# Optimization experiments

Hardware: AMD Instinct MI355X
Metric: run time of the kernel (lower is better)

Reference implementation:

```python
import jax, jax.numpy as jnp
import numpy as np

N = 50000   # nodes per branch
E = 500000  # edges per branch
B = 256     # graphs per batch
F = 320     # node feature dim = num_features_xd*10
H = 10      # GAT heads
C = 32      # GAT out channels per head
NEG_SLOPE = 0.2


def _seg_sum(x, idx, n):
    return jax.ops.segment_sum(x, idx, num_segments=n)


def gcn_conv(x, edge_index, W, b):
    n = x.shape[0]
    h = x @ W  # [N, F]
    loop = jnp.arange(n, dtype=edge_index.dtype)
    src = jnp.concatenate([edge_index[0], loop])
    dst = jnp.concatenate([edge_index[1], loop])
    deg = _seg_sum(jnp.ones_like(dst, dtype=h.dtype), dst, n)
    dinv = jnp.where(deg > 0, jax.lax.rsqrt(deg), 0.0)
    coef = (dinv[src] * dinv[dst])[:, None]  # [E+N, 1]
    out = _seg_sum(h[src] * coef, dst, n)
    return out + b


def gat_conv(x, edge_index, W, att_src, att_dst, b):
    # PyG GATConv, heads=H, concat=True, add_self_loops=True, negative_slope=0.2
    n = x.shape[0]
    h = (x @ W).reshape(n, H, C)  # [N, H, C]
    a_s = jnp.sum(h * att_src, axis=-1)  # [N, H]
    a_d = jnp.sum(h * att_dst, axis=-1)  # [N, H]
    loop = jnp.arange(n, dtype=edge_index.dtype)
    src = jnp.concatenate([edge_index[0], loop])
    dst = jnp.concatenate([edge_index[1], loop])
    e = jax.nn.leaky_relu(a_s[src] + a_d[dst], NEG_SLOPE)  # [E+N, H]
    m = jax.ops.segment_max(e, dst, num_segments=n)  # neighborhood max per head
    p = jnp.exp(e - m[dst])
    denom = _seg_sum(p, dst, n)  # [N, H], >0 thanks to self loops
    alpha = p / denom[dst]
    out = _seg_sum(h[src] * alpha[:, :, None], dst, n)  # [N, H, C]
    return out.reshape(n, H * C) + b


def graph_branch(x, edge_index, batch, params):
    x = jax.nn.relu(gcn_conv(x, edge_index, params['W_gcn'], params['b_gcn']))
    x = jax.nn.relu(gat_conv(x, edge_index, params['W_gat'], params['att_src'], params['att_dst'], params['b_gat']))
    gmp = jax.ops.segment_max(x, batch, num_segments=B)  # [B, F]
    cnt = _seg_sum(jnp.ones((x.shape[0], 1), x.dtype), batch, B)
    gap = _seg_sum(x, batch, B) / jnp.maximum(cnt, 1.0)
    g = jnp.concatenate([gmp, gap], axis=1)  # [B, 2F]
    g = jax.nn.relu(g @ params['W_fc_g1'] + params['b_fc_g1'])
    # dropout is identity in eval mode
    g = g @ params['W_fc_g2'] + params['b_fc_g2']
    return g


def _forward(x_a, x_b, edge_index_a, edge_index_b, batch_a, batch_b, params):
    ga = graph_branch(x_a, edge_index_a, batch_a, params)
    gb = graph_branch(x_b, edge_index_b, batch_b, params)
    xc = jnp.concatenate([ga, gb], axis=1)  # [B, 256]
    xc = jax.nn.relu(xc @ params['W_fc1'] + params['b_fc1'])
    xc = jax.nn.relu(xc @ params['W_fc2'] + params['b_fc2'])
    return xc @ params['W_out'] + params['b_out']  # [B, 2]


def setup_inputs() -> dict:
    key = jax.random.key(0)
    ks = jax.random.split(key, 24)
    s = 0.05
    d = {
        'x_a': jax.random.normal(ks[0], (N, F), jnp.float32),
        'x_b': jax.random.normal(ks[1], (N, F), jnp.float32),
        'edge_index_a': jax.random.randint(ks[2], (2, E), 0, N, jnp.int32),
        'edge_index_b': jax.random.randint(ks[3], (2, E), 0, N, jnp.int32),
        'batch_a': jnp.sort(jax.random.randint(ks[4], (N,), 0, B, jnp.int32)),
        'batch_b': jnp.sort(jax.random.randint(ks[5], (N,), 0, B, jnp.int32)),
        'W_gcn': jax.random.normal(ks[6], (F, F), jnp.float32) * s,
        'b_gcn': jax.random.normal(ks[7], (F,), jnp.float32) * s,
        'W_gat': jax.random.normal(ks[8], (F, H * C), jnp.float32) * s,
        'att_src': jax.random.normal(ks[9], (H, C), jnp.float32) * s,
        'att_dst': jax.random.normal(ks[10], (H, C), jnp.float32) * s,
        'b_gat': jax.random.normal(ks[11], (H * C,), jnp.float32) * s,
        'W_fc_g1': jax.random.normal(ks[12], (2 * F, 1500), jnp.float32) * s,
        'b_fc_g1': jax.random.normal(ks[13], (1500,), jnp.float32) * s,
        'W_fc_g2': jax.random.normal(ks[14], (1500, 128), jnp.float32) * s,
        'b_fc_g2': jax.random.normal(ks[15], (128,), jnp.float32) * s,
        'W_fc1': jax.random.normal(ks[16], (256, 1024), jnp.float32) * s,
        'b_fc1': jax.random.normal(ks[17], (1024,), jnp.float32) * s,
        'W_fc2': jax.random.normal(ks[18], (1024, 512), jnp.float32) * s,
        'b_fc2': jax.random.normal(ks[19], (512,), jnp.float32) * s,
        'W_out': jax.random.normal(ks[20], (512, 2), jnp.float32) * s,
        'b_out': jax.random.normal(ks[21], (2,), jnp.float32) * s,
    }
    return d


def reference(x_a, x_b, edge_index_a, edge_index_b, batch_a, batch_b,
              W_gcn, b_gcn, W_gat, att_src, att_dst, b_gat,
              W_fc_g1, b_fc_g1, W_fc_g2, b_fc_g2,
              W_fc1, b_fc1, W_fc2, b_fc2, W_out, b_out):
    params = dict(W_gcn=W_gcn, b_gcn=b_gcn, W_gat=W_gat, att_src=att_src,
                  att_dst=att_dst, b_gat=b_gat, W_fc_g1=W_fc_g1, b_fc_g1=b_fc_g1,
                  W_fc_g2=W_fc_g2, b_fc_g2=b_fc_g2, W_fc1=W_fc1, b_fc1=b_fc1,
                  W_fc2=W_fc2, b_fc2=b_fc2, W_out=W_out, b_out=b_out)
    return _forward(x_a, x_b, edge_index_a, edge_index_b, batch_a, batch_b, params)
```

## Files before the change

kernel.cpp:

```cpp
#include <hip/hip_runtime.h>
#include <type_traits>

#define FDIM 320
#define NHEADS 10
#define NGR 256

typedef __bf16 bf16x8 __attribute__((ext_vector_type(8)));
typedef float f32x4 __attribute__((ext_vector_type(4)));

__global__ void wconv2_kernel(const float* __restrict__ Wg, const float* __restrict__ Wa,
                              __bf16* __restrict__ Tg, __bf16* __restrict__ Ta) {
  int idx = blockIdx.x * 256 + threadIdx.x;
  bool first = idx < FDIM * FDIM;
  const float* W = first ? Wg : Wa;
  __bf16* T = first ? Tg : Ta;
  int i2 = first ? idx : idx - FDIM * FDIM;
  int k = i2 / FDIM, c = i2 - k * FDIM;
  T[c * FDIM + k] = (__bf16)W[i2];
}

#define GLSTR 40

template<typename TA, bool SCORES>
__global__ __launch_bounds__(256, 2) void gemm320v3_kernel(
    const TA* __restrict__ A, const TA* __restrict__ A2, int Npad, int Nreal,
    const __bf16* __restrict__ Wt, __bf16* __restrict__ C,
    const float* __restrict__ att_s, const float* __restrict__ att_d,
    float* __restrict__ as_, float* __restrict__ ad_)
{
  __shared__ __bf16 As[2][64 * GLSTR];
  __shared__ __bf16 Bs[2][320 * GLSTR];

  const int tid = threadIdx.x;
  const int lane = tid & 63;
  const int w = tid >> 6;
  const int wr = w >> 1, wc = w & 1;
  const int r = lane & 15, kg = lane >> 4;
  const int m0 = blockIdx.x * 64;
  const bool brB = m0 >= Npad;
  const int loff = brB ? Npad : 0;

  const int brow = tid >> 2, bq = tid & 3;
  const int grow = m0 + brow;
  const int lrow = grow - loff;
  const bool arow_ok = lrow < Nreal;

  bf16x8 bstg[5];
  bf16x8 astg;
  float4 af32a, af32b;

  auto stage_load = [&](int k0) {
    #pragma unroll
    for (int i = 0; i < 5; i++) {
      int ch = tid + i * 256;
      int col = ch >> 2, kc = ch & 3;
      bstg[i] = *(const bf16x8*)(Wt + (size_t)col * FDIM + k0 + kc * 8);
    }
    if constexpr (std::is_same_v<TA, float>) {
      if (arow_ok) {
        const float* Ab = brB ? A2 : A;
        const float4* ap = (const float4*)(Ab + (size_t)lrow * FDIM + k0 + bq * 8);
        af32a = ap[0]; af32b = ap[1];
      }
    } else {
      if (arow_ok) astg = *(const bf16x8*)(A + (size_t)grow * FDIM + k0 + bq * 8);
    }
  };
  auto stage_write = [&](int b) {
    #pragma unroll
    for (int i = 0; i < 5; i++) {
      int ch = tid + i * 256;
      int col = ch >> 2, kc = ch & 3;
      *(bf16x8*)&Bs[b][col * GLSTR + kc * 8] = bstg[i];
    }
    bf16x8 v = {};
    if constexpr (std::is_same_v<TA, float>) {
      if (arow_ok) {
        v[0]=(__bf16)af32a.x; v[1]=(__bf16)af32a.y; v[2]=(__bf16)af32a.z; v[3]=(__bf16)af32a.w;
        v[4]=(__bf16)af32b.x; v[5]=(__bf16)af32b.y; v[6]=(__bf16)af32b.z; v[7]=(__bf16)af32b.w;
      }
    } else {
      if (arow_ok) v = astg;
    }
    *(bf16x8*)&As[b][brow * GLSTR + bq * 8] = v;
  };

  f32x4 acc0[10], acc1[10];
  #pragma unroll
  for (int i = 0; i < 10; i++) { acc0[i] = (f32x4){0,0,0,0}; acc1[i] = (f32x4){0,0,0,0}; }

  stage_load(0);
  stage_write(0);
  __syncthreads();

  int cur = 0;
  for (int k = 0; k < 10; k++) {
    if (k < 9) stage_load((k + 1) * 32);
    {
      bf16x8 a0 = *(const bf16x8*)&As[cur][(wr*32 + r)      * GLSTR + kg*8];
      bf16x8 a1 = *(const bf16x8*)&As[cur][(wr*32 + 16 + r) * GLSTR + kg*8];
      #pragma unroll
      for (int nf = 0; nf < 10; nf++) {
        bf16x8 b = *(const bf16x8*)&Bs[cur][(wc*160 + nf*16 + r) * GLSTR + kg*8];
        acc0[nf] = __builtin_amdgcn_mfma_f32_16x16x32_bf16(a0, b, acc0[nf], 0, 0, 0);
        acc1[nf] = __builtin_amdgcn_mfma_f32_16x16x32_bf16(a1, b, acc1[nf], 0, 0, 0);
      }
    }
    if (k < 9) {
      stage_write(cur ^ 1);
      __syncthreads();
      cur ^= 1;
    }
  }

  #pragma unroll
  for (int nf = 0; nf < 10; nf++) {
    int gn = wc*160 + nf*16 + r;
    #pragma unroll
    for (int q = 0; q < 4; q++) {
      int gm0 = m0 + wr*32 + kg*4 + q;
      if (gm0 - loff < Nreal) C[(size_t)gm0 * FDIM + gn] = (__bf16)acc0[nf][q];
      int gm1 = gm0 + 16;
      if (gm1 - loff < Nreal) C[(size_t)gm1 * FDIM + gn] = (__bf16)acc1[nf][q];
    }
  }

  if constexpr (SCORES) {
    #pragma unroll
    for (int th = 0; th < 5; th++) {
      int t = wc * 5 + th;
      float s0 = att_s[t*32 + r],      s1 = att_s[t*32 + 16 + r];
      float d0 = att_d[t*32 + r],      d1 = att_d[t*32 + 16 + r];
      #pragma unroll
      for (int q = 0; q < 4; q++) {
        float ps0 = acc0[2*th][q]*s0 + acc0[2*th+1][q]*s1;
        float ps1 = acc1[2*th][q]*s0 + acc1[2*th+1][q]*s1;
        float pd0 = acc0[2*th][q]*d0 + acc0[2*th+1][q]*d1;
        float pd1 = acc1[2*th][q]*d0 + acc1[2*th+1][q]*d1;
        #pragma unroll
        for (int off = 1; off < 16; off <<= 1) {
          ps0 += __shfl_xor(ps0, off, 16);
          ps1 += __shfl_xor(ps1, off, 16);
          pd0 += __shfl_xor(pd0, off, 16);
          pd1 += __shfl_xor(pd1, off, 16);
        }
        if (r == 0) {
          int row0 = m0 + wr*32 + kg*4 + q;
          if (row0 - loff < Nreal) { as_[row0*NHEADS + t] = ps0; ad_[row0*NHEADS + t] = pd0; }
          int row1 = row0 + 16;
          if (row1 - loff < Nreal) { as_[row1*NHEADS + t] = ps1; ad_[row1*NHEADS + t] = pd1; }
        }
      }
    }
  }
}

#define BM 128
#define BN 64
#define BK 32
#define LSTR 56

template<int FLAGS>
__global__ __launch_bounds__(256) void gemm_bf16_kernel(
    const float* __restrict__ A, const float* __restrict__ B,
    float* __restrict__ C, const float* __restrict__ bias,
    int M, int N, int K, int ldc)
{
  __shared__ __bf16 As[BM * LSTR];
  __shared__ __bf16 Bs[BN * LSTR];

  const int tid = threadIdx.x;
  const int lane = tid & 63;
  const int w = tid >> 6;
  const int wm = w >> 1, wn = w & 1;
  const int r = lane & 15, kg = lane >> 4;
  const int m0 = blockIdx.x * BM, n0 = blockIdx.y * BN;

  f32x4 acc[4][2];
  #pragma unroll
  for (int i = 0; i < 4; i++)
    #pragma unroll
    for (int j = 0; j < 2; j++)
      acc[i][j] = (f32x4){0.f, 0.f, 0.f, 0.f};

  const int arow = tid >> 1, ahalf = tid & 1;
  const int bk = tid >> 3, bn = (tid & 7) * 8;

  for (int k0 = 0; k0 < K; k0 += BK) {
    __syncthreads();
    {
      int gm = m0 + arow;
      int kbase = k0 + ahalf * 16;
      float tmp[16];
      if (gm < M && kbase + 16 <= K) {
        const float4* ap = (const float4*)(A + (size_t)gm * K + kbase);
        #pragma unroll
        for (int q = 0; q < 4; q++) {
          float4 v = ap[q];
          tmp[q*4+0] = v.x; tmp[q*4+1] = v.y; tmp[q*4+2] = v.z; tmp[q*4+3] = v.w;
        }
      } else {
        #pragma unroll
        for (int q = 0; q < 16; q++) {
          int kk = kbase + q;
          tmp[q] = (gm < M && kk < K) ? A[(size_t)gm * K + kk] : 0.f;
        }
      }
      bf16x8 v0, v1;
      #pragma unroll
      for (int q = 0; q < 8; q++) { v0[q] = (__bf16)tmp[q]; v1[q] = (__bf16)tmp[q+8]; }
      bf16x8* dp = (bf16x8*)&As[arow * LSTR + ahalf * 16];
      dp[0] = v0; dp[1] = v1;
    }
    {
      int gk = k0 + bk;
      float tb[8];
      if (gk < K && n0 + bn + 8 <= N) {
        const float4* bp = (const float4*)(B + (size_t)gk * N + n0 + bn);
        float4 u0 = bp[0], u1 = bp[1];
        tb[0]=u0.x; tb[1]=u0.y; tb[2]=u0.z; tb[3]=u0.w;
        tb[4]=u1.x; tb[5]=u1.y; tb[6]=u1.z; tb[7]=u1.w;
      } else {
        #pragma unroll
        for (int q = 0; q < 8; q++) {
          int gn = n0 + bn + q;
          tb[q] = (gk < K && gn < N) ? B[(size_t)gk * N + gn] : 0.f;
        }
      }
      #pragma unroll
      for (int q = 0; q < 8; q++) Bs[(bn + q) * LSTR + bk] = (__bf16)tb[q];
    }
    __syncthreads();
    bf16x8 af[4], bfr[2];
    #pragma unroll
    for (int mf = 0; mf < 4; mf++)
      af[mf] = *(const bf16x8*)&As[(wm*64 + mf*16 + r) * LSTR + kg*8];
    #pragma unroll
    for (int nf = 0; nf < 2; nf++)
      bfr[nf] = *(const bf16x8*)&Bs[(wn*32 + nf*16 + r) * LSTR + kg*8];
    #pragma unroll
    for (int mf = 0; mf < 4; mf++)
      #pragma unroll
      for (int nf = 0; nf < 2; nf++)
        acc[mf][nf] = __builtin_amdgcn_mfma_f32_16x16x32_bf16(af[mf], bfr[nf], acc[mf][nf], 0, 0, 0);
  }

  #pragma unroll
  for (int mf = 0; mf < 4; mf++) {
    #pragma unroll
    for (int nf = 0; nf < 2; nf++) {
      #pragma unroll
      for (int q = 0; q < 4; q++) {
        int gm = m0 + wm*64 + mf*16 + kg*4 + q;
        int gn = n0 + wn*32 + nf*16 + r;
        if (gm < M && gn < N) {
          float v = acc[mf][nf][q];
          if (FLAGS & 2) v += bias[gn];
          if (FLAGS & 1) v = fmaxf(v, 0.f);
          C[(size_t)gm * ldc + gn] = v;
        }
      }
    }
  }
}

__global__ __launch_bounds__(256) void gemm_splitk_kernel(
    const float* __restrict__ A, const float* __restrict__ B,
    float* __restrict__ P, int M, int N, int K, int KS)
{
  __shared__ __bf16 As[BM * LSTR];
  __shared__ __bf16 Bs[BN * LSTR];

  const int tid = threadIdx.x;
  const int lane = tid & 63;
  const int w = tid >> 6;
  const int wm = w >> 1, wn = w & 1;
  const int r = lane & 15, kg = lane >> 4;
  const int m0 = blockIdx.x * BM, n0 = blockIdx.y * BN;
  const int kstart = blockIdx.z * KS;
  const int kend = min(K, kstart + KS);

  f32x4 acc[4][2];
  #pragma unroll
  for (int i = 0; i < 4; i++)
    #pragma unroll
    for (int j = 0; j < 2; j++)
      acc[i][j] = (f32x4){0.f, 0.f, 0.f, 0.f};

  const int arow = tid >> 1, ahalf = tid & 1;
  const int bk = tid >> 3, bn = (tid & 7) * 8;

  for (int k0 = kstart; k0 < kend; k0 += BK) {
    __syncthreads();
    {
      int gm = m0 + arow;
      int kbase = k0 + ahalf * 16;
      float tmp[16];
      if (gm < M && kbase + 16 <= kend) {
        const float4* ap = (const float4*)(A + (size_t)gm * K + kbase);
        #pragma unroll
        for (int q = 0; q < 4; q++) {
          float4 v = ap[q];
          tmp[q*4+0] = v.x; tmp[q*4+1] = v.y; tmp[q*4+2] = v.z; tmp[q*4+3] = v.w;
        }
      } else {
        #pragma unroll
        for (int q = 0; q < 16; q++) {
          int kk = kbase + q;
          tmp[q] = (gm < M && kk < kend) ? A[(size_t)gm * K + kk] : 0.f;
        }
      }
      bf16x8 v0, v1;
      #pragma unroll
      for (int q = 0; q < 8; q++) { v0[q] = (__bf16)tmp[q]; v1[q] = (__bf16)tmp[q+8]; }
      bf16x8* dp = (bf16x8*)&As[arow * LSTR + ahalf * 16];
      dp[0] = v0; dp[1] = v1;
    }
    {
      int gk = k0 + bk;
      float tb[8];
      if (gk < kend && n0 + bn + 8 <= N) {
        const float4* bp = (const float4*)(B + (size_t)gk * N + n0 + bn);
        float4 u0 = bp[0], u1 = bp[1];
        tb[0]=u0.x; tb[1]=u0.y; tb[2]=u0.z; tb[3]=u0.w;
        tb[4]=u1.x; tb[5]=u1.y; tb[6]=u1.z; tb[7]=u1.w;
      } else {
        #pragma unroll
        for (int q = 0; q < 8; q++) {
          int gn = n0 + bn + q;
          tb[q] = (gk < kend && gn < N) ? B[(size_t)gk * N + gn] : 0.f;
        }
      }
      #pragma unroll
      for (int q = 0; q < 8; q++) Bs[(bn + q) * LSTR + bk] = (__bf16)tb[q];
    }
    __syncthreads();
    bf16x8 af[4], bfr[2];
    #pragma unroll
    for (int mf = 0; mf < 4; mf++)
      af[mf] = *(const bf16x8*)&As[(wm*64 + mf*16 + r) * LSTR + kg*8];
    #pragma unroll
    for (int nf = 0; nf < 2; nf++)
      bfr[nf] = *(const bf16x8*)&Bs[(wn*32 + nf*16 + r) * LSTR + kg*8];
    #pragma unroll
    for (int mf = 0; mf < 4; mf++)
      #pragma unroll
      for (int nf = 0; nf < 2; nf++)
        acc[mf][nf] = __builtin_amdgcn_mfma_f32_16x16x32_bf16(af[mf], bfr[nf], acc[mf][nf], 0, 0, 0);
  }

  float* Pp = P + (size_t)blockIdx.z * M * N;
  #pragma unroll
  for (int mf = 0; mf < 4; mf++) {
    #pragma unroll
    for (int nf = 0; nf < 2; nf++) {
      #pragma unroll
      for (int q = 0; q < 4; q++) {
        int gm = m0 + wm*64 + mf*16 + kg*4 + q;
        int gn = n0 + wn*32 + nf*16 + r;
        if (gm < M && gn < N)
          Pp[(size_t)gm * N + gn] = acc[mf][nf][q];
      }
    }
  }
}

template<int FLAGS, bool STACK>
__global__ void reduce_kernel(const float* __restrict__ P, float* __restrict__ C,
                              const float* __restrict__ bias, int M, int N, int S, int ldc)
{
  int i = blockIdx.x * 256 + threadIdx.x;
  if (i >= M * N) return;
  float v = 0.f;
  for (int s = 0; s < S; s++) v += P[(size_t)s * M * N + i];
  int row = i / N, col = i - row * N;
  if (FLAGS & 2) v += bias[col];
  if (FLAGS & 1) v = fmaxf(v, 0.f);
  if (STACK) { if (row >= (M >> 1)) { row -= (M >> 1); col += N; } }
  C[(size_t)row * ldc + col] = v;
}

__global__ void count_kernel(const int* __restrict__ dst_a, const int* __restrict__ dst_b,
                             int* __restrict__ cnt, int E, int Npad) {
  int e = blockIdx.x * 256 + threadIdx.x;
  if (e < E) atomicAdd(&cnt[dst_a[e]], 1);
  else if (e < 2 * E) atomicAdd(&cnt[dst_b[e - E] + Npad], 1);
}

__global__ void bsum_kernel(const int* __restrict__ cnt, int* __restrict__ bsum, int n) {
  __shared__ int wp[4];
  int tid = threadIdx.x, lane = tid & 63, wid = tid >> 6;
  int i = blockIdx.x * 256 + tid;
  int v = (i < n) ? cnt[i] : 0;
  #pragma unroll
  for (int off = 32; off >= 1; off >>= 1) v += __shfl_xor(v, off, 64);
  if (lane == 0) wp[wid] = v;
  __syncthreads();
  if (tid == 0) bsum[blockIdx.x] = wp[0] + wp[1] + wp[2] + wp[3];
}

__global__ __launch_bounds__(1024) void bscan_kernel(int* __restrict__ bsum, int nb) {
  __shared__ int wp[16];
  int tid = threadIdx.x, lane = tid & 63, wid = tid >> 6;
  int v = (tid < nb) ? bsum[tid] : 0;
  int xv = v;
  #pragma unroll
  for (int off = 1; off < 64; off <<= 1) {
    int y = __shfl_up(xv, off, 64);
    if (lane >= off) xv += y;
  }
  if (lane == 63) wp[wid] = xv;
  __syncthreads();
  if (tid == 0) { int s = 0; for (int k = 0; k < 16; k++) { int t = wp[k]; wp[k] = s; s += t; } }
  __syncthreads();
  if (tid < nb) bsum[tid] = wp[wid] + xv - v;
}

__global__ void rpfill_kernel(const int* __restrict__ cnt, const int* __restrict__ bsum,
                              int* __restrict__ rp, float* __restrict__ dinv, int n, int E2) {
  __shared__ int wp[4];
  int tid = threadIdx.x, lane = tid & 63, wid = tid >> 6;
  int i = blockIdx.x * 256 + tid;
  int v = (i < n) ? cnt[i] : 0;
  int xv = v;
  #pragma unroll
  for (int off = 1; off < 64; off <<= 1) {
    int y = __shfl_up(xv, off, 64);
    if (lane >= off) xv += y;
  }
  if (lane == 63) wp[wid] = xv;
  __syncthreads();
  if (tid == 0) { int s = 0; for (int k = 0; k < 4; k++) { int t = wp[k]; wp[k] = s; s += t; } }
  __syncthreads();
  if (i < n) {
    rp[i] = bsum[blockIdx.x] + wp[wid] + xv - v;
    dinv[i] = rsqrtf((float)(v + 1));
  }
  if (blockIdx.x == 0 && tid == 0) rp[n] = E2;
}

__global__ void fill_kernel(const int* __restrict__ sa, const int* __restrict__ da,
                            const int* __restrict__ sb, const int* __restrict__ db,
                            const int* __restrict__ rp, int* __restrict__ fil,
                            int* __restrict__ csr, int E, int Npad) {
  int e = blockIdx.x * 256 + threadIdx.x;
  if (e >= 2 * E) return;
  int s, d;
  if (e < E) { s = sa[e]; d = da[e]; }
  else       { s = sb[e - E] + Npad; d = db[e - E] + Npad; }
  int pos = rp[d] + atomicAdd(&fil[d], 1);
  csr[pos] = s;
}

__global__ void gcn_agg_kernel(const __bf16* __restrict__ h, const int* __restrict__ rp,
                               const int* __restrict__ csr, const float* __restrict__ dinv,
                               const float* __restrict__ bias, __bf16* __restrict__ out,
                               int n2, int Npad, int Nreal)
{
  const int lane = threadIdx.x & 63;
  int v0 = blockIdx.x * 4 + (threadIdx.x >> 6);
  if (v0 >= n2) return;
  const int v = __builtin_amdgcn_readfirstlane(v0);
  const int lv = (v >= Npad) ? v - Npad : v;
  if (lv >= Nreal) return;
  const bool act = lane < 40;
  const float dv = dinv[v];
  const int e0 = rp[v], e1 = rp[v + 1];
  float acc[8], bia[8];
  if (act) {
    bf16x8 hv = *(const bf16x8*)(h + (size_t)v * FDIM + 8 * lane);
    const float4* bp = (const float4*)(bias + 8 * lane);
    float4 b0 = bp[0], b1 = bp[1];
    bia[0]=b0.x; bia[1]=b0.y; bia[2]=b0.z; bia[3]=b0.w;
    bia[4]=b1.x; bia[5]=b1.y; bia[6]=b1.z; bia[7]=b1.w;
    #pragma unroll
    for (int j = 0; j < 8; j++) acc[j] = dv * (float)hv[j];
  }
  int e = e0;
  for (; e + 4 <= e1; e += 4) {
    int sj0 = csr[e], sj1 = csr[e+1], sj2 = csr[e+2], sj3 = csr[e+3];
    float c0 = dinv[sj0], c1 = dinv[sj1], c2 = dinv[sj2], c3 = dinv[sj3];
    if (act) {
      bf16x8 h0 = *(const bf16x8*)(h + (size_t)sj0 * FDIM + 8 * lane);
      bf16x8 h1 = *(const bf16x8*)(h + (size_t)sj1 * FDIM + 8 * lane);
      bf16x8 h2 = *(const bf16x8*)(h + (size_t)sj2 * FDIM + 8 * lane);
      bf16x8 h3 = *(const bf16x8*)(h + (size_t)sj3 * FDIM + 8 * lane);
      #pragma unroll
      for (int j = 0; j < 8; j++)
        acc[j] += c0 * (float)h0[j] + c1 * (float)h1[j]
                + c2 * (float)h2[j] + c3 * (float)h3[j];
    }
  }
  for (; e < e1; e++) {
    int sj = csr[e];
    float cj = dinv[sj];
    if (act) {
      bf16x8 hv = *(const bf16x8*)(h + (size_t)sj * FDIM + 8 * lane);
      #pragma unroll
      for (int j = 0; j < 8; j++) acc[j] += cj * (float)hv[j];
    }
  }
  if (act) {
    bf16x8 o;
    #pragma unroll
    for (int j = 0; j < 8; j++) o[j] = (__bf16)fmaxf(dv * acc[j] + bia[j], 0.f);
    *(bf16x8*)(out + (size_t)v * FDIM + 8 * lane) = o;
  }
}

__device__ __forceinline__ float lrelu(float x) { return x > 0.f ? x : 0.2f * x; }

__global__ void mdenom4_kernel(const int* __restrict__ rp, const int* __restrict__ csr,
                               const float* __restrict__ as_, const float* __restrict__ ad_,
                               float* __restrict__ aint, float* __restrict__ aself,
                               int n2, int Npad, int Nreal)
{
  int tid = blockIdx.x * 256 + threadIdx.x;
  if (tid >= n2 * NHEADS) return;
  int v = tid / NHEADS, t = tid - v * NHEADS;
  int lv = (v >= Npad) ? v - Npad : v;
  if (lv >= Nreal) return;
  int e0 = rp[v], e1 = rp[v + 1];
  float adv = ad_[tid];
  float esf = lrelu(as_[tid] + adv);
  float m = esf, den = 1.f;
  for (int e = e0; e < e1; e++) {
    int s = csr[e];
    float ev = lrelu(as_[s * NHEADS + t] + adv);
    float nm = fmaxf(m, ev);
    den = den * __expf(m - nm) + __expf(ev - nm);
    m = nm;
  }
  float inv = 1.f / den;
  for (int e = e0; e < e1; e++) {
    int s = csr[e];
    aint[(size_t)e * NHEADS + t] = __expf(lrelu(as_[s * NHEADS + t] + adv) - m) * inv;
  }
  aself[tid] = __expf(esf - m) * inv;
}

__global__ void gat_agg_kernel(const __bf16* __restrict__ h, const int* __restrict__ rp,
                               const int* __restrict__ csr, const float* __restrict__ aint,
                               const float* __restrict__ aself, const float* __restrict__ bias,
                               __bf16* __restrict__ out, int n2, int Npad, int Nreal)
{
  const int lane = threadIdx.x & 63;
  int v0 = blockIdx.x * 4 + (threadIdx.x >> 6);
  if (v0 >= n2) return;
  const int v = __builtin_amdgcn_readfirstlane(v0);
  const int lv = (v >= Npad) ? v - Npad : v;
  if (lv >= Nreal) return;
  const bool act = lane < 40;
  const int hl = lane >> 2;
  const int e0 = rp[v], e1 = rp[v + 1];

  float acc[8], bia[8];
  if (act) {
    float aslf = aself[v * NHEADS + hl];
    bf16x8 hv = *(const bf16x8*)(h + (size_t)v * FDIM + 8 * lane);
    const float4* bp = (const float4*)(bias + 8 * lane);
    float4 b0 = bp[0], b1 = bp[1];
    bia[0]=b0.x; bia[1]=b0.y; bia[2]=b0.z; bia[3]=b0.w;
    bia[4]=b1.x; bia[5]=b1.y; bia[6]=b1.z; bia[7]=b1.w;
    #pragma unroll
    for (int j = 0; j < 8; j++) acc[j] = aslf * (float)hv[j];
  }

  int e = e0;
  for (; e + 4 <= e1; e += 4) {
    int sj0 = csr[e], sj1 = csr[e+1], sj2 = csr[e+2], sj3 = csr[e+3];
    if (act) {
      float a0 = aint[(size_t)(e+0) * NHEADS + hl];
      float a1 = aint[(size_t)(e+1) * NHEADS + hl];
      float a2 = aint[(size_t)(e+2) * NHEADS + hl];
      float a3 = aint[(size_t)(e+3) * NHEADS + hl];
      bf16x8 h0 = *(const bf16x8*)(h + (size_t)sj0 * FDIM + 8 * lane);
      bf16x8 h1 = *(const bf16x8*)(h + (size_t)sj1 * FDIM + 8 * lane);
      bf16x8 h2 = *(const bf16x8*)(h + (size_t)sj2 * FDIM + 8 * lane);
      bf16x8 h3 = *(const bf16x8*)(h + (size_t)sj3 * FDIM + 8 * lane);
      #pragma unroll
      for (int j = 0; j < 8; j++)
        acc[j] += a0 * (float)h0[j] + a1 * (float)h1[j]
                + a2 * (float)h2[j] + a3 * (float)h3[j];
    }
  }
  for (; e < e1; e++) {
    int sj = csr[e];
    if (act) {
      float al = aint[(size_t)e * NHEADS + hl];
      bf16x8 hv = *(const bf16x8*)(h + (size_t)sj * FDIM + 8 * lane);
      #pragma unroll
      for (int j = 0; j < 8; j++) acc[j] += al * (float)hv[j];
    }
  }
  if (act) {
    bf16x8 o;
    #pragma unroll
    for (int j = 0; j < 8; j++) o[j] = (__bf16)fmaxf(acc[j] + bia[j], 0.f);
    *(bf16x8*)(out + (size_t)v * FDIM + 8 * lane) = o;
  }
}

__global__ void bstart_kernel(const int* __restrict__ ba, const int* __restrict__ bb,
                              int* __restrict__ bst, int n, int Npad) {
  int idx = blockIdx.x * 256 + threadIdx.x;
  if (idx >= 2 * (n + 1)) return;
  int br = idx >= (n + 1);
  int v = idx - br * (n + 1);
  const int* batch = br ? bb : ba;
  int off = br ? Npad : 0;
  int* bs = bst + br * (NGR + 1);
  int bv = (v < n) ? batch[v] : NGR;
  int bp = (v == 0) ? -1 : batch[v - 1];
  for (int gg = bp + 1; gg <= bv; gg++) bs[gg] = v + off;
}

__global__ __launch_bounds__(256) void pool_kernel(
    const __bf16* __restrict__ xin, const int* __restrict__ bstart,
    float* __restrict__ g)
{
  __shared__ float pmx[4][FDIM];
  __shared__ float psm[4][FDIM];
  const int gid = blockIdx.x;
  const int br = gid >= NGR;
  const int lg = gid - br * NGR;
  const int* bs = bstart + br * (NGR + 1);
  const int lane = threadIdx.x & 63;
  const int wid = threadIdx.x >> 6;
  const bool act = lane < 40;
  const int s = bs[lg], e = bs[lg + 1];
  float mx[8], sm[8];
  #pragma unroll
  for (int j = 0; j < 8; j++) { mx[j] = -__builtin_inff(); sm[j] = 0.f; }
  for (int v = s + wid; v < e; v += 4) {
    if (act) {
      bf16x8 hv = *(const bf16x8*)(xin + (size_t)v * FDIM + 8 * lane);
      #pragma unroll
      for (int j = 0; j < 8; j++) {
        float val = (float)hv[j];
        mx[j] = fmaxf(mx[j], val);
        sm[j] += val;
      }
    }
  }
  if (act) {
    #pragma unroll
    for (int j = 0; j < 8; j++) {
      pmx[wid][8 * lane + j] = mx[j];
      psm[wid][8 * lane + j] = sm[j];
    }
  }
  __syncthreads();
  if (wid == 0 && act) {
    float cntf = (float)(e - s);
    float rcnt = 1.f / fmaxf(cntf, 1.f);
    #pragma unroll
    for (int j = 0; j < 8; j++) {
      int c = 8 * lane + j;
      float m2 = fmaxf(fmaxf(pmx[0][c], pmx[1][c]), fmaxf(pmx[2][c], pmx[3][c]));
      float s2 = psm[0][c] + psm[1][c] + psm[2][c] + psm[3][c];
      g[gid * (2 * FDIM) + c] = m2;
      g[gid * (2 * FDIM) + FDIM + c] = s2 * rcnt;
    }
  }
}

extern "C" void kernel_launch(void* const* d_in, const int* in_sizes, int n_in,
                              void* d_out, int out_size, void* d_ws, size_t ws_size,
                              hipStream_t stream)
{
  const int N = in_sizes[0] / FDIM;
  const int E = in_sizes[2] / 2;
  const int Npad = (N + 63) & ~63;
  const int n2 = 2 * Npad;
  const int NB2 = (n2 + 255) / 256;

  const float* x_a = (const float*)d_in[0];
  const float* x_b = (const float*)d_in[1];
  const int*   ei_a = (const int*)d_in[2];
  const int*   ei_b = (const int*)d_in[3];
  const int*   bat_a = (const int*)d_in[4];
  const int*   bat_b = (const int*)d_in[5];
  const float* W_gcn   = (const float*)d_in[6];
  const float* b_gcn   = (const float*)d_in[7];
  const float* W_gat   = (const float*)d_in[8];
  const float* att_src = (const float*)d_in[9];
  const float* att_dst = (const float*)d_in[10];
  const float* b_gat   = (const float*)d_in[11];
  const float* W_fc_g1 = (const float*)d_in[12];
  const float* b_fc_g1 = (const float*)d_in[13];
  const float* W_fc_g2 = (const float*)d_in[14];
  const float* b_fc_g2 = (const float*)d_in[15];
  const float* W_fc1   = (const float*)d_in[16];
  const float* b_fc1   = (const float*)d_in[17];
  const float* W_fc2   = (const float*)d_in[18];
  const float* b_fc2   = (const float*)d_in[19];
  const float* W_out   = (const float*)d_in[20];
  const float* b_out   = (const float*)d_in[21];
  float* outp = (float*)d_out;

  char* ws = (char*)d_ws;
  size_t off = 0;
  auto alloc = [&](size_t bytes) -> char* {
    char* p = ws + off;
    off += (bytes + 255) & ~(size_t)255;
    return p;
  };
  int*    cnt    = (int*)alloc((size_t)n2 * 4);
  int*    fil    = (int*)alloc((size_t)n2 * 4);
  size_t  zero_span = (size_t)((char*)fil - (char*)cnt) + (((size_t)n2 * 4 + 255) & ~(size_t)255);
  int*    rp     = (int*)alloc((size_t)(n2 + 1) * 4);
  int*    bsum   = (int*)alloc((size_t)NB2 * 4);
  int*    csr    = (int*)alloc((size_t)2 * E * 4);
  float*  dinv   = (float*)alloc((size_t)n2 * 4);
  int*    bstart = (int*)alloc((size_t)2 * (NGR + 1) * 4);
  __bf16* WgcnT  = (__bf16*)alloc((size_t)FDIM * FDIM * 2);
  __bf16* WgatT  = (__bf16*)alloc((size_t)FDIM * FDIM * 2);
  __bf16* hbuf   = (__bf16*)alloc((size_t)n2 * FDIM * 2);
  __bf16* xbuf   = (__bf16*)alloc((size_t)n2 * FDIM * 2);
  float*  as_    = (float*)alloc((size_t)n2 * NHEADS * 4);
  float*  ad_    = (float*)alloc((size_t)n2 * NHEADS * 4);
  float*  aself  = (float*)alloc((size_t)n2 * NHEADS * 4);
  size_t aint_bytes = (size_t)2 * E * NHEADS * 4;
  size_t part_bytes = (size_t)8 * 512 * 512 * 4;
  float*  aint   = (float*)alloc(aint_bytes > part_bytes ? aint_bytes : part_bytes);
  float*  part   = aint;
  float*  g      = (float*)alloc((size_t)2 * NGR * 2 * FDIM * 4);
  float*  t1     = (float*)alloc((size_t)2 * NGR * 1500 * 4);
  float*  xc     = (float*)alloc((size_t)NGR * 256 * 4);
  float*  t2     = (float*)alloc((size_t)NGR * 1024 * 4);
  float*  t3     = (float*)alloc((size_t)NGR * 512 * 4);
  if (off > ws_size) return;

  wconv2_kernel<<<2 * (FDIM * FDIM) / 256, 256, 0, stream>>>(W_gcn, W_gat, WgcnT, WgatT);

  hipMemsetAsync(cnt, 0, zero_span, stream);
  count_kernel<<<(2 * E + 255) / 256, 256, 0, stream>>>(ei_a + E, ei_b + E, cnt, E, Npad);
  bsum_kernel<<<NB2, 256, 0, stream>>>(cnt, bsum, n2);
  bscan_kernel<<<1, 1024, 0, stream>>>(bsum, NB2);
  rpfill_kernel<<<NB2, 256, 0, stream>>>(cnt, bsum, rp, dinv, n2, 2 * E);
  fill_kernel<<<(2 * E + 255) / 256, 256, 0, stream>>>(ei_a, ei_a + E, ei_b, ei_b + E,
                                                       rp, fil, csr, E, Npad);

  int g320 = n2 / 64;
  gemm320v3_kernel<float, false><<<g320, 256, 0, stream>>>(
      x_a, x_b, Npad, N, WgcnT, hbuf, nullptr, nullptr, nullptr, nullptr);
  gcn_agg_kernel<<<(n2 + 3) / 4, 256, 0, stream>>>(hbuf, rp, csr, dinv, b_gcn, xbuf, n2, Npad, N);
  gemm320v3_kernel<__bf16, true><<<g320, 256, 0, stream>>>(
      xbuf, nullptr, Npad, N, WgatT, hbuf, att_src, att_dst, as_, ad_);

  mdenom4_kernel<<<(n2 * NHEADS + 255) / 256, 256, 0, stream>>>(rp, csr, as_, ad_, aint, aself, n2, Npad, N);
  gat_agg_kernel<<<(n2 + 3) / 4, 256, 0, stream>>>(hbuf, rp, csr, aint, aself, b_gat, xbuf, n2, Npad, N);

  bstart_kernel<<<(2 * (N + 1) + 255) / 256, 256, 0, stream>>>(bat_a, bat_b, bstart, N, Npad);
  pool_kernel<<<2 * NGR, 256, 0, stream>>>(xbuf, bstart, g);

  {
    dim3 gfc1((512 + BM - 1) / BM, (1500 + BN - 1) / BN);
    gemm_bf16_kernel<3><<<gfc1, 256, 0, stream>>>(g, W_fc_g1, t1, b_fc_g1, 512, 1500, 2 * FDIM, 1500);
    int S = 8, KS = ((1500 + S * BK - 1) / (S * BK)) * BK;
    dim3 gfc2((512 + BM - 1) / BM, (128 + BN - 1) / BN, S);
    gemm_splitk_kernel<<<gfc2, 256, 0, stream>>>(t1, W_fc_g2, part, 512, 128, 1500, KS);
    reduce_kernel<2, true><<<(512 * 128 + 255) / 256, 256, 0, stream>>>(part, xc, b_fc_g2, 512, 128, S, 256);
  }
  {
    dim3 gx1((NGR + BM - 1) / BM, (1024 + BN - 1) / BN);
    gemm_bf16_kernel<3><<<gx1, 256, 0, stream>>>(xc, W_fc1, t2, b_fc1, NGR, 1024, 256, 1024);
    int S = 4, KS = ((1024 + S * BK - 1) / (S * BK)) * BK;
    dim3 gx2((NGR + BM - 1) / BM, (512 + BN - 1) / BN, S);
    gemm_splitk_kernel<<<gx2, 256, 0, stream>>>(t2, W_fc2, part, NGR, 512, 1024, KS);
    reduce_kernel<3, false><<<(NGR * 512 + 255) / 256, 256, 0, stream>>>(part, t3, b_fc2, NGR, 512, S, 512);
    int S2 = 4, KS2 = ((512 + S2 * BK - 1) / (S2 * BK)) * BK;
    dim3 gx3((NGR + BM - 1) / BM, 1, S2);
    gemm_splitk_kernel<<<gx3, 256, 0, stream>>>(t3, W_out, part, NGR, 2, 512, KS2);
    reduce_kernel<2, false><<<(NGR * 2 + 255) / 256, 256, 0, stream>>>(part, outp, b_out, NGR, 2, S2, 2);
  }
}
```

Before: 612.1 us.

## Drop softmax max pass in GAT and fuse prep kernels into one launch

The GAT softmax kernel now makes a single pass over each node's edges. It stores unnormalized exp scores and a per-node inverse denominator instead of first computing the running max and then a second normalization pass, and the aggregation kernel applies the inverse denominator at the end. Separately, weight transpose/convert, edge in-degree counting and graph-start computation are merged into one kernel launch, which saves launch overhead. Dropping the max subtraction risks exp overflow when the attention logits are large.

Result: faster. 591.9 us (-3.3%).

```diff
diff --git a/kernel.cpp b/kernel.cpp
--- a/kernel.cpp
+++ b/kernel.cpp
@@ -8,15 +8,39 @@
 typedef __bf16 bf16x8 __attribute__((ext_vector_type(8)));
 typedef float f32x4 __attribute__((ext_vector_type(4)));
 
-__global__ void wconv2_kernel(const float* __restrict__ Wg, const float* __restrict__ Wa,
-                              __bf16* __restrict__ Tg, __bf16* __restrict__ Ta) {
-  int idx = blockIdx.x * 256 + threadIdx.x;
-  bool first = idx < FDIM * FDIM;
-  const float* W = first ? Wg : Wa;
-  __bf16* T = first ? Tg : Ta;
-  int i2 = first ? idx : idx - FDIM * FDIM;
-  int k = i2 / FDIM, c = i2 - k * FDIM;
-  T[c * FDIM + k] = (__bf16)W[i2];
+__global__ void prep_kernel(const float* __restrict__ Wg, const float* __restrict__ Wa,
+                            __bf16* __restrict__ Tg, __bf16* __restrict__ Ta,
+                            const int* __restrict__ dst_a, const int* __restrict__ dst_b,
+                            int* __restrict__ cnt, int E,
+                            const int* __restrict__ ba, const int* __restrict__ bb,
+                            int* __restrict__ bst, int n, int Npad,
+                            int nbW, int nbC)
+{
+  int b = blockIdx.x;
+  if (b < nbW) {
+    int idx = b * 256 + threadIdx.x;
+    bool first = idx < FDIM * FDIM;
+    const float* W = first ? Wg : Wa;
+    __bf16* T = first ? Tg : Ta;
+    int i2 = first ? idx : idx - FDIM * FDIM;
+    int k = i2 / FDIM, c = i2 - k * FDIM;
+    T[c * FDIM + k] = (__bf16)W[i2];
+  } else if (b < nbW + nbC) {
+    int e = (b - nbW) * 256 + threadIdx.x;
+    if (e < E) atomicAdd(&cnt[dst_a[e]], 1);
+    else if (e < 2 * E) atomicAdd(&cnt[dst_b[e - E] + Npad], 1);
+  } else {
+    int idx = (b - nbW - nbC) * 256 + threadIdx.x;
+    if (idx >= 2 * (n + 1)) return;
+    int br = idx >= (n + 1);
+    int v = idx - br * (n + 1);
+    const int* batch = br ? bb : ba;
+    int off2 = br ? Npad : 0;
+    int* bs = bst + br * (NGR + 1);
+    int bv = (v < n) ? batch[v] : NGR;
+    int bp = (v == 0) ? -1 : batch[v - 1];
+    for (int gg = bp + 1; gg <= bv; gg++) bs[gg] = v + off2;
+  }
 }
 
 #define GLSTR 40
@@ -378,13 +402,6 @@
   if (FLAGS & 1) v = fmaxf(v, 0.f);
   if (STACK) { if (row >= (M >> 1)) { row -= (M >> 1); col += N; } }
   C[(size_t)row * ldc + col] = v;
-}
-
-__global__ void count_kernel(const int* __restrict__ dst_a, const int* __restrict__ dst_b,
-                             int* __restrict__ cnt, int E, int Npad) {
-  int e = blockIdx.x * 256 + threadIdx.x;
-  if (e < E) atomicAdd(&cnt[dst_a[e]], 1);
-  else if (e < 2 * E) atomicAdd(&cnt[dst_b[e - E] + Npad], 1);
 }
 
 __global__ void bsum_kernel(const int* __restrict__ cnt, int* __restrict__ bsum, int n) {
@@ -510,10 +527,10 @@
 
 __device__ __forceinline__ float lrelu(float x) { return x > 0.f ? x : 0.2f * x; }
 
-__global__ void mdenom4_kernel(const int* __restrict__ rp, const int* __restrict__ csr,
+__global__ void mdenom5_kernel(const int* __restrict__ rp, const int* __restrict__ csr,
                                const float* __restrict__ as_, const float* __restrict__ ad_,
                                float* __restrict__ aint, float* __restrict__ aself,
-                               int n2, int Npad, int Nreal)
+                               float* __restrict__ invden, int n2, int Npad, int Nreal)
 {
   int tid = blockIdx.x * 256 + threadIdx.x;
   if (tid >= n2 * NHEADS) return;
@@ -522,27 +539,23 @@
   if (lv >= Nreal) return;
   int e0 = rp[v], e1 = rp[v + 1];
   float adv = ad_[tid];
-  float esf = lrelu(as_[tid] + adv);
-  float m = esf, den = 1.f;
+  float pself = __expf(lrelu(as_[tid] + adv));
+  float den = pself;
   for (int e = e0; e < e1; e++) {
     int s = csr[e];
-    float ev = lrelu(as_[s * NHEADS + t] + adv);
-    float nm = fmaxf(m, ev);
-    den = den * __expf(m - nm) + __expf(ev - nm);
-    m = nm;
-  }
-  float inv = 1.f / den;
-  for (int e = e0; e < e1; e++) {
-    int s = csr[e];
-    aint[(size_t)e * NHEADS + t] = __expf(lrelu(as_[s * NHEADS + t] + adv) - m) * inv;
-  }
-  aself[tid] = __expf(esf - m) * inv;
+    float p = __expf(lrelu(as_[s * NHEADS + t] + adv));
+    aint[(size_t)e * NHEADS + t] = p;
+    den += p;
+  }
+  aself[tid] = pself;
+  invden[tid] = 1.f / den;
 }
 
 __global__ void gat_agg_kernel(const __bf16* __restrict__ h, const int* __restrict__ rp,
                                const int* __restrict__ csr, const float* __restrict__ aint,
-                               const float* __restrict__ aself, const float* __restrict__ bias,
-                               __bf16* __restrict__ out, int n2, int Npad, int Nreal)
+                               const float* __restrict__ aself, const float* __restrict__ invden,
+                               const float* __restrict__ bias, __bf16* __restrict__ out,
+                               int n2, int Npad, int Nreal)
 {
   const int lane = threadIdx.x & 63;
   int v0 = blockIdx.x * 4 + (threadIdx.x >> 6);
@@ -554,9 +567,10 @@
   const int hl = lane >> 2;
   const int e0 = rp[v], e1 = rp[v + 1];
 
-  float acc[8], bia[8];
+  float acc[8], bia[8], inv_t = 0.f;
   if (act) {
     float aslf = aself[v * NHEADS + hl];
+    inv_t = invden[v * NHEADS + hl];
     bf16x8 hv = *(const bf16x8*)(h + (size_t)v * FDIM + 8 * lane);
     const float4* bp = (const float4*)(bias + 8 * lane);
     float4 b0 = bp[0], b1 = bp[1];
@@ -596,23 +610,9 @@
   if (act) {
     bf16x8 o;
     #pragma unroll
-    for (int j = 0; j < 8; j++) o[j] = (__bf16)fmaxf(acc[j] + bia[j], 0.f);
+    for (int j = 0; j < 8; j++) o[j] = (__bf16)fmaxf(acc[j] * inv_t + bia[j], 0.f);
     *(bf16x8*)(out + (size_t)v * FDIM + 8 * lane) = o;
   }
-}
-
-__global__ void bstart_kernel(const int* __restrict__ ba, const int* __restrict__ bb,
-                              int* __restrict__ bst, int n, int Npad) {
-  int idx = blockIdx.x * 256 + threadIdx.x;
-  if (idx >= 2 * (n + 1)) return;
-  int br = idx >= (n + 1);
-  int v = idx - br * (n + 1);
-  const int* batch = br ? bb : ba;
-  int off = br ? Npad : 0;
-  int* bs = bst + br * (NGR + 1);
-  int bv = (v < n) ? batch[v] : NGR;
-  int bp = (v == 0) ? -1 : batch[v - 1];
-  for (int gg = bp + 1; gg <= bv; gg++) bs[gg] = v + off;
 }
 
 __global__ __launch_bounds__(256) void pool_kernel(
@@ -721,6 +721,7 @@
   float*  as_    = (float*)alloc((size_t)n2 * NHEADS * 4);
   float*  ad_    = (float*)alloc((size_t)n2 * NHEADS * 4);
   float*  aself  = (float*)alloc((size_t)n2 * NHEADS * 4);
+  float*  invden = (float*)alloc((size_t)n2 * NHEADS * 4);
   size_t aint_bytes = (size_t)2 * E * NHEADS * 4;
   size_t part_bytes = (size_t)8 * 512 * 512 * 4;
   float*  aint   = (float*)alloc(aint_bytes > part_bytes ? aint_bytes : part_bytes);
@@ -732,10 +733,15 @@
   float*  t3     = (float*)alloc((size_t)NGR * 512 * 4);
   if (off > ws_size) return;
 
-  wconv2_kernel<<<2 * (FDIM * FDIM) / 256, 256, 0, stream>>>(W_gcn, W_gat, WgcnT, WgatT);
-
   hipMemsetAsync(cnt, 0, zero_span, stream);
-  count_kernel<<<(2 * E + 255) / 256, 256, 0, stream>>>(ei_a + E, ei_b + E, cnt, E, Npad);
+  {
+    int nbW = 2 * (FDIM * FDIM) / 256;
+    int nbC = (2 * E + 255) / 256;
+    int nbB = (2 * (N + 1) + 255) / 256;
+    prep_kernel<<<nbW + nbC + nbB, 256, 0, stream>>>(
+        W_gcn, W_gat, WgcnT, WgatT, ei_a + E, ei_b + E, cnt, E,
+        bat_a, bat_b, bstart, N, Npad, nbW, nbC);
+  }
   bsum_kernel<<<NB2, 256, 0, stream>>>(cnt, bsum, n2);
   bscan_kernel<<<1, 1024, 0, stream>>>(bsum, NB2);
   rpfill_kernel<<<NB2, 256, 0, stream>>>(cnt, bsum, rp, dinv, n2, 2 * E);
@@ -749,10 +755,11 @@
   gemm320v3_kernel<__bf16, true><<<g320, 256, 0, stream>>>(
       xbuf, nullptr, Npad, N, WgatT, hbuf, att_src, att_dst, as_, ad_);
 
-  mdenom4_kernel<<<(n2 * NHEADS + 255) / 256, 256, 0, stream>>>(rp, csr, as_, ad_, aint, aself, n2, Npad, N);
-  gat_agg_kernel<<<(n2 + 3) / 4, 256, 0, stream>>>(hbuf, rp, csr, aint, aself, b_gat, xbuf, n2, Npad, N);
-
-  bstart_kernel<<<(2 * (N + 1) + 255) / 256, 256, 0, stream>>>(bat_a, bat_b, bstart, N, Npad);
+  mdenom5_kernel<<<(n2 * NHEADS + 255) / 256, 256, 0, stream>>>(
+      rp, csr, as_, ad_, aint, aself, invden, n2, Npad, N);
+  gat_agg_kernel<<<(n2 + 3) / 4, 256, 0, stream>>>(
+      hbuf, rp, csr, aint, aself, invden, b_gat, xbuf, n2, Npad, N);
+
   pool_kernel<<<2 * NGR, 256, 0, stream>>>(xbuf, bstart, g);
 
   {
```
